# Optimization experiments

Measured on AMD Instinct MI355X. Metric: run time of the kernel, lower is better.

## Reference

```python
import jax, jax.numpy as jnp
import numpy as np
from jax import lax

GROUPS = 4
NEG_INF = -1000000000.0


def setup_inputs() -> dict:
    key = jax.random.key(0)
    k1, k2, k3 = jax.random.split(key, 3)
    B, C, L, K = 2, 16, 2048, 11
    scores = jax.random.normal(k1, (B, C, L, L), dtype=jnp.float32)
    weight = jax.random.normal(k2, (C, C // GROUPS, K, K), dtype=jnp.float32) * 0.05
    bias = jax.random.normal(k3, (C,), dtype=jnp.float32) * 0.05
    return {"scores": scores, "weight": weight, "bias": bias}


def reference(scores, weight, bias):
    B, C, L, _ = scores.shape
    K = weight.shape[-1]
    pad = K // 2
    # causal (lower-triangular) mask over the L x L score map
    mask = jnp.tril(jnp.ones((L, L), dtype=bool))[None, None]  # [1,1,L,L]
    neg_inf = jnp.asarray(NEG_INF, dtype=scores.dtype)
    s_inf = jnp.where(mask, scores, neg_inf)
    probs = jax.nn.softmax(s_inf, axis=-1)
    # grouped conv2d over the attention-probability maps, same padding
    out = lax.conv_general_dilated(
        probs, weight,
        window_strides=(1, 1),
        padding=[(pad, pad), (pad, pad)],
        dimension_numbers=("NCHW", "OIHW", "NCHW"),
        feature_group_count=GROUPS,
    )
    out = out + bias[None, :, None, None]
    # re-mask: zero out the upper triangle
    return jnp.where(mask, out, jnp.zeros((), dtype=out.dtype))
```

## Files before the change

kernel.cpp:

```cpp
#include <hip/hip_runtime.h>
#include <cmath>

#define L_DIM 2048
#define C_CH  16
#define B_SZ  2
#define N_G   4
#define C_PG  4
#define K_SZ  11

#define BX 64
#define BY 128
#define CHY 16
#define QROWS 31
#define QPITCH 84
#define QROWB (QPITCH*8)
#define NUNIT (QROWS*42)
#define NU 6
#define CXC 80
#define MP 52
#define CLWB (CXC*MP*2)

typedef _Float16 f16;
typedef __attribute__((ext_vector_type(2))) __fp16 fp16x2;
typedef __attribute__((ext_vector_type(8))) _Float16 f16x8;
typedef __attribute__((ext_vector_type(4))) float f32x4;
typedef unsigned long long u64;

struct alignas(8) H4 { f16 x, y, z, w; };
union H8U { H4 h[2]; uint4 u; };

__global__ void pack_w_k(const float* __restrict__ weight, u64* __restrict__ qprobs) {
  for (int e = threadIdx.x; e < 1536; e += 256) {
    const int l  = e & 63;
    const int r1 = e >> 6;
    const int t  = r1 % 3;
    const int r2 = r1 / 3;
    const int s  = r2 & 1;
    const int g  = r2 >> 1;
    const int m  = 16 * t + (l & 15);
    const int q  = l >> 4;
    const int kx = m >> 2, co = m & 3;
    f16 vals[8];
#pragma unroll
    for (int j = 0; j < 8; ++j) {
      const int ci = j & 3;
      const int ky = 8 * s + 2 * q + (j >> 2);
      float wv = 0.f;
      if (kx < K_SZ && ky < K_SZ)
        wv = weight[(((size_t)(g * 4 + co) * C_PG + ci) * K_SZ + ky) * K_SZ + kx];
      vals[j] = (f16)wv;
    }
    f16* dst = reinterpret_cast<f16*>(
        reinterpret_cast<char*>(qprobs) +
        ((size_t)(g * 2 + s) * L_DIM + 512) * 8 + (size_t)(t * 64 + l) * 16);
#pragma unroll
    for (int j = 0; j < 8; ++j) dst[j] = vals[j];
  }
}

__global__ __launch_bounds__(256) void softmax_q_k(
    const float* __restrict__ scores, u64* __restrict__ qprobs) {
  const int bid = blockIdx.x;
  const int zg  = bid & 7;
  const int y   = bid >> 3;
  const int b   = zg >> 2, g = zg & 3;
  const int tid = threadIdx.x;
  const int w    = tid >> 6;
  const int lane = tid & 63;

  __shared__ float mred[4][4];
  __shared__ float sred[4][4];

  const float* sbase = scores + ((size_t)(b * C_CH + g * 4) * L_DIM + y) * L_DIM;
  const size_t plane = (size_t)L_DIM * L_DIM;

  float v[4][8];
#pragma unroll
  for (int cc = 0; cc < 4; ++cc)
#pragma unroll
    for (int j = 0; j < 4; ++j) {
      const int x = 512 * w + 128 * j + 2 * lane;
      float2 f = make_float2(-INFINITY, -INFINITY);
      if (512 * w + 128 * j <= y) {
        f = *reinterpret_cast<const float2*>(sbase + cc * plane + x);
        if (x > y)     f.x = -INFINITY;
        if (x + 1 > y) f.y = -INFINITY;
      }
      v[cc][2 * j]     = f.x;
      v[cc][2 * j + 1] = f.y;
    }

  float ml[4];
#pragma unroll
  for (int cc = 0; cc < 4; ++cc) {
    float m = v[cc][0];
#pragma unroll
    for (int i = 1; i < 8; ++i) m = fmaxf(m, v[cc][i]);
#pragma unroll
    for (int off = 32; off >= 1; off >>= 1) m = fmaxf(m, __shfl_xor(m, off, 64));
    ml[cc] = m;
  }
  if (lane == 0) {
#pragma unroll
    for (int cc = 0; cc < 4; ++cc) mred[w][cc] = ml[cc];
  }
  __syncthreads();
  float mf[4];
#pragma unroll
  for (int cc = 0; cc < 4; ++cc)
    mf[cc] = fmaxf(fmaxf(mred[0][cc], mred[1][cc]),
                   fmaxf(mred[2][cc], mred[3][cc]));

  float sl[4];
#pragma unroll
  for (int cc = 0; cc < 4; ++cc) {
    float s = 0.f;
#pragma unroll
    for (int i = 0; i < 8; ++i) { v[cc][i] = __expf(v[cc][i] - mf[cc]); s += v[cc][i]; }
#pragma unroll
    for (int off = 32; off >= 1; off >>= 1) s += __shfl_xor(s, off, 64);
    sl[cc] = s;
  }
  if (lane == 0) {
#pragma unroll
    for (int cc = 0; cc < 4; ++cc) sred[w][cc] = sl[cc];
  }
  __syncthreads();
  float inv[4];
#pragma unroll
  for (int cc = 0; cc < 4; ++cc)
    inv[cc] = 1.0f / (sred[0][cc] + sred[1][cc] + sred[2][cc] + sred[3][cc]);

  u64* qrow = qprobs + ((size_t)zg * L_DIM + y) * L_DIM;
#pragma unroll
  for (int j = 0; j < 4; ++j) {
    const int xbase = 512 * w + 128 * j;
    if (xbase > y + 11) continue;
    const int x = xbase + 2 * lane;
    H8U o;
    o.h[0].x = (f16)(v[0][2*j]   * inv[0]);
    o.h[0].y = (f16)(v[1][2*j]   * inv[1]);
    o.h[0].z = (f16)(v[2][2*j]   * inv[2]);
    o.h[0].w = (f16)(v[3][2*j]   * inv[3]);
    o.h[1].x = (f16)(v[0][2*j+1] * inv[0]);
    o.h[1].y = (f16)(v[1][2*j+1] * inv[1]);
    o.h[1].z = (f16)(v[2][2*j+1] * inv[2]);
    o.h[1].w = (f16)(v[3][2*j+1] * inv[3]);
    *reinterpret_cast<uint4*>(qrow + x) = o.u;
  }
}

__global__ __launch_bounds__(256, 3) void conv_k(
    const u64* __restrict__ qprobs, const float* __restrict__ bias,
    float* __restrict__ out) {
  const int bid = blockIdx.x;
  const int zg  = bid & 7;
  const int lin = bid >> 3;
  const int xt  = lin & 31, yt = lin >> 5;
  const int x0 = xt * BX;
  const int Y0 = yt * BY;
  const int bb = zg >> 2, g = zg & 3;
  const int tid = threadIdx.x;
  const size_t plane = (size_t)L_DIM * L_DIM;

  float* outg = out + (size_t)(bb * C_CH + g * 4) * plane;

  if (x0 >= Y0 + BY) {
    const int co = (tid >> 4) & 3;
    const int xq = tid & 15;
    const float4 z4 = make_float4(0.f, 0.f, 0.f, 0.f);
    for (int r = (tid >> 6); r < BY; r += 4) {
      float* op = outg + (size_t)co * plane + (size_t)(Y0 + r) * L_DIM + x0 + 4 * xq;
      *reinterpret_cast<float4*>(op) = z4;
    }
    return;
  }

  __shared__ u64 Qs[QROWS * QPITCH];
  __shared__ f16 CLs[4 * CXC * MP];

  const int lane = tid & 63;
  const int w    = tid >> 6;
  const int q    = lane >> 4;
  const int c    = lane & 15;

  f16x8 A00, A01, A10, A11, A20, A21;
  {
    const char* qp0 = reinterpret_cast<const char*>(qprobs);
    const char* at0 = qp0 + ((size_t)(g * 2 + 0) * L_DIM + 512) * 8;
    const char* at1 = qp0 + ((size_t)(g * 2 + 1) * L_DIM + 512) * 8;
    A00 = *reinterpret_cast<const f16x8*>(at0 + (0 * 64 + lane) * 16);
    A10 = *reinterpret_cast<const f16x8*>(at0 + (1 * 64 + lane) * 16);
    A20 = *reinterpret_cast<const f16x8*>(at0 + (2 * 64 + lane) * 16);
    A01 = *reinterpret_cast<const f16x8*>(at1 + (0 * 64 + lane) * 16);
    A11 = *reinterpret_cast<const f16x8*>(at1 + (1 * 64 + lane) * 16);
    A21 = *reinterpret_cast<const f16x8*>(at1 + (2 * 64 + lane) * 16);
  }

  const float bs0 = bias[g * 4 + 0], bs1 = bias[g * 4 + 1];
  const float bs2 = bias[g * 4 + 2], bs3 = bias[g * 4 + 3];

  const u64* qplane = qprobs + (size_t)zg * plane;
  const int qx0 = x0 - 8;

  char* const qbase = reinterpret_cast<char*>(Qs);
  char* const clw   = reinterpret_cast<char*>(CLs) + w * CLWB;
  const char* const qlane = qbase + q * 1344 + c * 8;
  char* const clwr  = clw + c * 104 + q * 8;
  const char* const cle = clw + (lane + 3) * 104;

  for (int cb = Y0; cb < Y0 + BY; cb += CHY) {
    if (x0 > cb + CHY - 1) {
      const int co = (tid >> 4) & 3;
      const int xq = tid & 15;
      const float4 z4 = make_float4(0.f, 0.f, 0.f, 0.f);
      for (int r = (tid >> 6); r < CHY; r += 4) {
        float* op = outg + (size_t)co * plane + (size_t)(cb + r) * L_DIM + x0 + 4 * xq;
        *reinterpret_cast<float4*>(op) = z4;
      }
      continue;
    }

    uint4 sv[NU];
#pragma unroll
    for (int k = 0; k < NU; ++k) {
      const int u   = tid + 256 * k;
      const int r   = u / 42;
      const int c16 = u - 42 * r;
      const int py  = cb - 5 + r;
      const int qc0 = qx0 + 2 * c16;
      sv[k] = make_uint4(0u, 0u, 0u, 0u);
      if (u < NUNIT && py >= 0 && py < L_DIM && qc0 >= 0 && qc0 <= L_DIM - 2)
        sv[k] = *reinterpret_cast<const uint4*>(qplane + (size_t)py * L_DIM + qc0);
    }
    __syncthreads();
#pragma unroll
    for (int k = 0; k < NU; ++k) {
      const int u   = tid + 256 * k;
      if (u < NUNIT) {
        const int r   = u / 42;
        const int c16 = u - 42 * r;
        *reinterpret_cast<uint4*>(qbase + r * QROWB + c16 * 16) = sv[k];
      }
    }
    __syncthreads();

    for (int i = 0; i < CHY / 4; ++i) {
      const int y = cb + w * (CHY / 4) + i;
      float* orow = outg + (size_t)y * L_DIM + x0 + lane;
      if (y < x0) {
        orow[0] = 0.f; orow[plane] = 0.f;
        orow[2 * plane] = 0.f; orow[3 * plane] = 0.f;
        continue;
      }
      const char* qy = qlane + (y - cb) * QROWB;

      u64 b00[5], b01[5], b10[5], b11[5];
#pragma unroll
      for (int xs = 0; xs < 5; ++xs) {
        b00[xs] = *reinterpret_cast<const u64*>(qy + xs * 128 + 0);
        b01[xs] = *reinterpret_cast<const u64*>(qy + xs * 128 + 672);
        b10[xs] = *reinterpret_cast<const u64*>(qy + xs * 128 + 5376);
        b11[xs] = *reinterpret_cast<const u64*>(qy + xs * 128 + 6048);
      }

#pragma unroll
      for (int xs = 0; xs < 5; ++xs) {
        union { u64 u[2]; f16x8 v; } B0, B1;
        B0.u[0] = b00[xs]; B0.u[1] = b01[xs];
        B1.u[0] = b10[xs]; B1.u[1] = b11[xs];
        f32x4 z = {0.f, 0.f, 0.f, 0.f};
        f32x4 c0 = __builtin_amdgcn_mfma_f32_16x16x32_f16(A00, B0.v, z, 0, 0, 0);
        c0 = __builtin_amdgcn_mfma_f32_16x16x32_f16(A01, B1.v, c0, 0, 0, 0);
        f32x4 c1 = __builtin_amdgcn_mfma_f32_16x16x32_f16(A10, B0.v, z, 0, 0, 0);
        c1 = __builtin_amdgcn_mfma_f32_16x16x32_f16(A11, B1.v, c1, 0, 0, 0);
        f32x4 c2 = __builtin_amdgcn_mfma_f32_16x16x32_f16(A20, B0.v, z, 0, 0, 0);
        c2 = __builtin_amdgcn_mfma_f32_16x16x32_f16(A21, B1.v, c2, 0, 0, 0);

        union { fp16x2 h[2]; u64 u; } pk;
        pk.h[0] = __builtin_amdgcn_cvt_pkrtz(c0[0], c0[1]);
        pk.h[1] = __builtin_amdgcn_cvt_pkrtz(c0[2], c0[3]);
        *reinterpret_cast<u64*>(clwr + xs * 1664 + 0) = pk.u;
        pk.h[0] = __builtin_amdgcn_cvt_pkrtz(c1[0], c1[1]);
        pk.h[1] = __builtin_amdgcn_cvt_pkrtz(c1[2], c1[3]);
        *reinterpret_cast<u64*>(clwr + xs * 1664 + 32) = pk.u;
        pk.h[0] = __builtin_amdgcn_cvt_pkrtz(c2[0], c2[1]);
        pk.h[1] = __builtin_amdgcn_cvt_pkrtz(c2[2], c2[3]);
        *reinterpret_cast<u64*>(clwr + xs * 1664 + 64) = pk.u;
      }

      float s0 = 0.f, s1 = 0.f, s2 = 0.f, s3 = 0.f;
#pragma unroll
      for (int kx = 0; kx < K_SZ; ++kx) {
        union { u64 u; f16 h[4]; } cv;
        cv.u = *reinterpret_cast<const u64*>(cle + kx * 112);
        s0 += (float)cv.h[0]; s1 += (float)cv.h[1];
        s2 += (float)cv.h[2]; s3 += (float)cv.h[3];
      }
      const bool act = (x0 + lane) <= y;
      orow[0]         = act ? s0 + bs0 : 0.f;
      orow[plane]     = act ? s1 + bs1 : 0.f;
      orow[2 * plane] = act ? s2 + bs2 : 0.f;
      orow[3 * plane] = act ? s3 + bs3 : 0.f;
    }
  }
}

extern "C" void kernel_launch(void* const* d_in, const int* in_sizes, int n_in,
                              void* d_out, int out_size, void* d_ws, size_t ws_size,
                              hipStream_t stream) {
  const float* scores = (const float*)d_in[0];
  const float* weight = (const float*)d_in[1];
  const float* bias   = (const float*)d_in[2];
  float* outp = (float*)d_out;
  u64* qprobs = (u64*)d_ws;

  pack_w_k<<<1, 256, 0, stream>>>(weight, qprobs);

  softmax_q_k<<<B_SZ * N_G * L_DIM, 256, 0, stream>>>(scores, qprobs);

  conv_k<<<(L_DIM / BX) * (L_DIM / BY) * B_SZ * N_G, 256, 0, stream>>>(
      qprobs, bias, outp);
}
```

Measured before the change: 396.6 us.

## Store conv partials diagonally in LDS and reduce with vector loads in fp16

Changes the LDS layout of the per-wave MFMA partial results so each output column's 11 kx contributions sit contiguously along a skewed (diagonal) row. The epilogue can then gather them with a few wide 16-byte loads instead of 11 strided 8-byte loads, and sums them with packed fp16 adds. It also skips the redundant third-tile store for one lane quadrant and raises wave priority around the MFMA block. The trade-off is that accumulation in fp16 rather than fp32 loses precision.

```diff
diff --git a/kernel.cpp b/kernel.cpp
--- a/kernel.cpp
+++ b/kernel.cpp
@@ -16,9 +16,8 @@
 #define QROWB (QPITCH*8)
 #define NUNIT (QROWS*42)
 #define NU 6
-#define CXC 80
-#define MP 52
-#define CLWB (CXC*MP*2)
+#define DROWS 91
+#define DROWB 88
 
 typedef _Float16 f16;
 typedef __attribute__((ext_vector_type(2))) __fp16 fp16x2;
@@ -28,6 +27,9 @@
 
 struct alignas(8) H4 { f16 x, y, z, w; };
 union H8U { H4 h[2]; uint4 u; };
+union U32H2 { unsigned u; fp16x2 h; };
+
+__device__ __forceinline__ fp16x2 h2u(unsigned x) { U32H2 t; t.u = x; return t.h; }
 
 __global__ void pack_w_k(const float* __restrict__ weight, u64* __restrict__ qprobs) {
   for (int e = threadIdx.x; e < 1536; e += 256) {
@@ -177,7 +179,7 @@
   }
 
   __shared__ u64 Qs[QROWS * QPITCH];
-  __shared__ f16 CLs[4 * CXC * MP];
+  __shared__ u64 CLd[4 * DROWS * (DROWB/8)];
 
   const int lane = tid & 63;
   const int w    = tid >> 6;
@@ -204,10 +206,10 @@
   const int qx0 = x0 - 8;
 
   char* const qbase = reinterpret_cast<char*>(Qs);
-  char* const clw   = reinterpret_cast<char*>(CLs) + w * CLWB;
+  char* const clw   = reinterpret_cast<char*>(CLd) + w * (DROWS * DROWB);
   const char* const qlane = qbase + q * 1344 + c * 8;
-  char* const clwr  = clw + c * 104 + q * 8;
-  const char* const cle = clw + (lane + 3) * 104;
+  char* const cw = clw + (c - q + 11) * DROWB + q * 8;
+  const char* const ce = clw + (lane + 14) * DROWB;
 
   for (int cb = Y0; cb < Y0 + BY; cb += CHY) {
     if (x0 > cb + CHY - 1) {
@@ -236,7 +238,7 @@
     __syncthreads();
 #pragma unroll
     for (int k = 0; k < NU; ++k) {
-      const int u   = tid + 256 * k;
+      const int u = tid + 256 * k;
       if (u < NUNIT) {
         const int r   = u / 42;
         const int c16 = u - 42 * r;
@@ -264,6 +266,7 @@
         b11[xs] = *reinterpret_cast<const u64*>(qy + xs * 128 + 6048);
       }
 
+      __builtin_amdgcn_s_setprio(1);
 #pragma unroll
       for (int xs = 0; xs < 5; ++xs) {
         union { u64 u[2]; f16x8 v; } B0, B1;
@@ -280,28 +283,38 @@
         union { fp16x2 h[2]; u64 u; } pk;
         pk.h[0] = __builtin_amdgcn_cvt_pkrtz(c0[0], c0[1]);
         pk.h[1] = __builtin_amdgcn_cvt_pkrtz(c0[2], c0[3]);
-        *reinterpret_cast<u64*>(clwr + xs * 1664 + 0) = pk.u;
+        *reinterpret_cast<u64*>(cw + xs * 1408 + 0)   = pk.u;
         pk.h[0] = __builtin_amdgcn_cvt_pkrtz(c1[0], c1[1]);
         pk.h[1] = __builtin_amdgcn_cvt_pkrtz(c1[2], c1[3]);
-        *reinterpret_cast<u64*>(clwr + xs * 1664 + 32) = pk.u;
-        pk.h[0] = __builtin_amdgcn_cvt_pkrtz(c2[0], c2[1]);
-        pk.h[1] = __builtin_amdgcn_cvt_pkrtz(c2[2], c2[3]);
-        *reinterpret_cast<u64*>(clwr + xs * 1664 + 64) = pk.u;
-      }
-
-      float s0 = 0.f, s1 = 0.f, s2 = 0.f, s3 = 0.f;
-#pragma unroll
-      for (int kx = 0; kx < K_SZ; ++kx) {
-        union { u64 u; f16 h[4]; } cv;
-        cv.u = *reinterpret_cast<const u64*>(cle + kx * 112);
-        s0 += (float)cv.h[0]; s1 += (float)cv.h[1];
-        s2 += (float)cv.h[2]; s3 += (float)cv.h[3];
-      }
+        *reinterpret_cast<u64*>(cw + xs * 1408 - 320) = pk.u;
+        if (q != 3) {
+          pk.h[0] = __builtin_amdgcn_cvt_pkrtz(c2[0], c2[1]);
+          pk.h[1] = __builtin_amdgcn_cvt_pkrtz(c2[2], c2[3]);
+          *reinterpret_cast<u64*>(cw + xs * 1408 - 640) = pk.u;
+        }
+      }
+      __builtin_amdgcn_s_setprio(0);
+
+      const uint4 r0 = *reinterpret_cast<const uint4*>(ce + 0);
+      const uint4 r1 = *reinterpret_cast<const uint4*>(ce + 16);
+      const uint4 r2 = *reinterpret_cast<const uint4*>(ce + 32);
+      const uint4 r3 = *reinterpret_cast<const uint4*>(ce + 48);
+      const uint4 r4 = *reinterpret_cast<const uint4*>(ce + 64);
+      const uint2 r5 = *reinterpret_cast<const uint2*>(ce + 80);
+      fp16x2 e01 = (h2u(r0.x) + h2u(r0.z)) + (h2u(r1.x) + h2u(r1.z));
+      fp16x2 f01 = (h2u(r2.x) + h2u(r2.z)) + (h2u(r3.x) + h2u(r3.z));
+      fp16x2 g01 = (h2u(r4.x) + h2u(r4.z)) + h2u(r5.x);
+      e01 = (e01 + f01) + g01;
+      fp16x2 e23 = (h2u(r0.y) + h2u(r0.w)) + (h2u(r1.y) + h2u(r1.w));
+      fp16x2 f23 = (h2u(r2.y) + h2u(r2.w)) + (h2u(r3.y) + h2u(r3.w));
+      fp16x2 g23 = (h2u(r4.y) + h2u(r4.w)) + h2u(r5.y);
+      e23 = (e23 + f23) + g23;
+
       const bool act = (x0 + lane) <= y;
-      orow[0]         = act ? s0 + bs0 : 0.f;
-      orow[plane]     = act ? s1 + bs1 : 0.f;
-      orow[2 * plane] = act ? s2 + bs2 : 0.f;
-      orow[3 * plane] = act ? s3 + bs3 : 0.f;
+      orow[0]         = act ? (float)e01[0] + bs0 : 0.f;
+      orow[plane]     = act ? (float)e01[1] + bs1 : 0.f;
+      orow[2 * plane] = act ? (float)e23[0] + bs2 : 0.f;
+      orow[3 * plane] = act ? (float)e23[1] + bs3 : 0.f;
     }
   }
 }
```

Result: slower. 454.0 us (+14.5%).

## Load conv B operands directly from global memory, dropping LDS staging and barriers

Applied to the files above, without the earlier changes.

The conv kernel no longer stages a 31-row halo tile of packed probabilities into shared memory with two block barriers per 16-row chunk. Each wave now owns 32 consecutive output rows and loads its MFMA B operands straight from global memory, with a bounds-checked fallback for edge tiles. Launch bounds move from 3 to 4 blocks per CU now that LDS use is smaller. The trade is about 2.5x redundant global/L2 traffic from overlapping halo rows across row iterations, and uncoalesced 8-byte loads in place of 16-byte cooperative loads.

```diff
diff --git a/kernel.cpp b/kernel.cpp
--- a/kernel.cpp
+++ b/kernel.cpp
@@ -10,12 +10,6 @@
 
 #define BX 64
 #define BY 128
-#define CHY 16
-#define QROWS 31
-#define QPITCH 84
-#define QROWB (QPITCH*8)
-#define NUNIT (QROWS*42)
-#define NU 6
 #define CXC 80
 #define MP 52
 #define CLWB (CXC*MP*2)
@@ -150,7 +144,14 @@
   }
 }
 
-__global__ __launch_bounds__(256, 3) void conv_k(
+__device__ __forceinline__ u64 ldq(const u64* __restrict__ qplane, int row, int col) {
+  u64 v = 0;
+  if (((unsigned)row < (unsigned)L_DIM) && ((unsigned)col < (unsigned)L_DIM))
+    v = qplane[((size_t)row << 11) + col];
+  return v;
+}
+
+__global__ __launch_bounds__(256, 4) void conv_k(
     const u64* __restrict__ qprobs, const float* __restrict__ bias,
     float* __restrict__ out) {
   const int bid = blockIdx.x;
@@ -176,7 +177,6 @@
     return;
   }
 
-  __shared__ u64 Qs[QROWS * QPITCH];
   __shared__ f16 CLs[4 * CXC * MP];
 
   const int lane = tid & 63;
@@ -203,106 +203,81 @@
   const u64* qplane = qprobs + (size_t)zg * plane;
   const int qx0 = x0 - 8;
 
-  char* const qbase = reinterpret_cast<char*>(Qs);
-  char* const clw   = reinterpret_cast<char*>(CLs) + w * CLWB;
-  const char* const qlane = qbase + q * 1344 + c * 8;
-  char* const clwr  = clw + c * 104 + q * 8;
+  char* const clw  = reinterpret_cast<char*>(CLs) + w * CLWB;
+  char* const clwr = clw + c * 104 + q * 8;
   const char* const cle = clw + (lane + 3) * 104;
 
-  for (int cb = Y0; cb < Y0 + BY; cb += CHY) {
-    if (x0 > cb + CHY - 1) {
-      const int co = (tid >> 4) & 3;
-      const int xq = tid & 15;
-      const float4 z4 = make_float4(0.f, 0.f, 0.f, 0.f);
-      for (int r = (tid >> 6); r < CHY; r += 4) {
-        float* op = outg + (size_t)co * plane + (size_t)(cb + r) * L_DIM + x0 + 4 * xq;
-        *reinterpret_cast<float4*>(op) = z4;
+  const bool fastB = (x0 >= 8) && (x0 + 72 <= L_DIM);
+
+  for (int i = 0; i < 32; ++i) {
+    const int y = Y0 + 32 * w + i;
+    float* orow = outg + (size_t)y * L_DIM + x0 + lane;
+    if (y < x0) {
+      orow[0] = 0.f; orow[plane] = 0.f;
+      orow[2 * plane] = 0.f; orow[3 * plane] = 0.f;
+      continue;
+    }
+
+    u64 b00[5], b01[5], b10[5], b11[5];
+    const int py0 = y - 5 + 2 * q;
+    if (fastB && y <= L_DIM - 11) {
+      const u64* p0 = qplane + ((size_t)py0 << 11) + (qx0 + c);
+#pragma unroll
+      for (int xs = 0; xs < 5; ++xs) {
+        b00[xs] = p0[16 * xs];
+        b01[xs] = p0[16 * xs + 2048];
+        b10[xs] = p0[16 * xs + 16384];
+        b11[xs] = p0[16 * xs + 18432];
       }
-      continue;
-    }
-
-    uint4 sv[NU];
-#pragma unroll
-    for (int k = 0; k < NU; ++k) {
-      const int u   = tid + 256 * k;
-      const int r   = u / 42;
-      const int c16 = u - 42 * r;
-      const int py  = cb - 5 + r;
-      const int qc0 = qx0 + 2 * c16;
-      sv[k] = make_uint4(0u, 0u, 0u, 0u);
-      if (u < NUNIT && py >= 0 && py < L_DIM && qc0 >= 0 && qc0 <= L_DIM - 2)
-        sv[k] = *reinterpret_cast<const uint4*>(qplane + (size_t)py * L_DIM + qc0);
-    }
-    __syncthreads();
-#pragma unroll
-    for (int k = 0; k < NU; ++k) {
-      const int u   = tid + 256 * k;
-      if (u < NUNIT) {
-        const int r   = u / 42;
-        const int c16 = u - 42 * r;
-        *reinterpret_cast<uint4*>(qbase + r * QROWB + c16 * 16) = sv[k];
+    } else {
+#pragma unroll
+      for (int xs = 0; xs < 5; ++xs) {
+        const int col = qx0 + 16 * xs + c;
+        b00[xs] = ldq(qplane, py0,     col);
+        b01[xs] = ldq(qplane, py0 + 1, col);
+        b10[xs] = ldq(qplane, py0 + 8, col);
+        b11[xs] = ldq(qplane, py0 + 9, col);
       }
     }
-    __syncthreads();
-
-    for (int i = 0; i < CHY / 4; ++i) {
-      const int y = cb + w * (CHY / 4) + i;
-      float* orow = outg + (size_t)y * L_DIM + x0 + lane;
-      if (y < x0) {
-        orow[0] = 0.f; orow[plane] = 0.f;
-        orow[2 * plane] = 0.f; orow[3 * plane] = 0.f;
-        continue;
-      }
-      const char* qy = qlane + (y - cb) * QROWB;
-
-      u64 b00[5], b01[5], b10[5], b11[5];
-#pragma unroll
-      for (int xs = 0; xs < 5; ++xs) {
-        b00[xs] = *reinterpret_cast<const u64*>(qy + xs * 128 + 0);
-        b01[xs] = *reinterpret_cast<const u64*>(qy + xs * 128 + 672);
-        b10[xs] = *reinterpret_cast<const u64*>(qy + xs * 128 + 5376);
-        b11[xs] = *reinterpret_cast<const u64*>(qy + xs * 128 + 6048);
-      }
-
-#pragma unroll
-      for (int xs = 0; xs < 5; ++xs) {
-        union { u64 u[2]; f16x8 v; } B0, B1;
-        B0.u[0] = b00[xs]; B0.u[1] = b01[xs];
-        B1.u[0] = b10[xs]; B1.u[1] = b11[xs];
-        f32x4 z = {0.f, 0.f, 0.f, 0.f};
-        f32x4 c0 = __builtin_amdgcn_mfma_f32_16x16x32_f16(A00, B0.v, z, 0, 0, 0);
-        c0 = __builtin_amdgcn_mfma_f32_16x16x32_f16(A01, B1.v, c0, 0, 0, 0);
-        f32x4 c1 = __builtin_amdgcn_mfma_f32_16x16x32_f16(A10, B0.v, z, 0, 0, 0);
-        c1 = __builtin_amdgcn_mfma_f32_16x16x32_f16(A11, B1.v, c1, 0, 0, 0);
-        f32x4 c2 = __builtin_amdgcn_mfma_f32_16x16x32_f16(A20, B0.v, z, 0, 0, 0);
-        c2 = __builtin_amdgcn_mfma_f32_16x16x32_f16(A21, B1.v, c2, 0, 0, 0);
-
-        union { fp16x2 h[2]; u64 u; } pk;
-        pk.h[0] = __builtin_amdgcn_cvt_pkrtz(c0[0], c0[1]);
-        pk.h[1] = __builtin_amdgcn_cvt_pkrtz(c0[2], c0[3]);
-        *reinterpret_cast<u64*>(clwr + xs * 1664 + 0) = pk.u;
-        pk.h[0] = __builtin_amdgcn_cvt_pkrtz(c1[0], c1[1]);
-        pk.h[1] = __builtin_amdgcn_cvt_pkrtz(c1[2], c1[3]);
-        *reinterpret_cast<u64*>(clwr + xs * 1664 + 32) = pk.u;
-        pk.h[0] = __builtin_amdgcn_cvt_pkrtz(c2[0], c2[1]);
-        pk.h[1] = __builtin_amdgcn_cvt_pkrtz(c2[2], c2[3]);
-        *reinterpret_cast<u64*>(clwr + xs * 1664 + 64) = pk.u;
-      }
-
-      float s0 = 0.f, s1 = 0.f, s2 = 0.f, s3 = 0.f;
-#pragma unroll
-      for (int kx = 0; kx < K_SZ; ++kx) {
-        union { u64 u; f16 h[4]; } cv;
-        cv.u = *reinterpret_cast<const u64*>(cle + kx * 112);
-        s0 += (float)cv.h[0]; s1 += (float)cv.h[1];
-        s2 += (float)cv.h[2]; s3 += (float)cv.h[3];
-      }
-      const bool act = (x0 + lane) <= y;
-      orow[0]         = act ? s0 + bs0 : 0.f;
-      orow[plane]     = act ? s1 + bs1 : 0.f;
-      orow[2 * plane] = act ? s2 + bs2 : 0.f;
-      orow[3 * plane] = act ? s3 + bs3 : 0.f;
-    }
+
+#pragma unroll
+    for (int xs = 0; xs < 5; ++xs) {
+      union { u64 u[2]; f16x8 v; } B0, B1;
+      B0.u[0] = b00[xs]; B0.u[1] = b01[xs];
+      B1.u[0] = b10[xs]; B1.u[1] = b11[xs];
+      f32x4 z = {0.f, 0.f, 0.f, 0.f};
+      f32x4 c0 = __builtin_amdgcn_mfma_f32_16x16x32_f16(A00, B0.v, z, 0, 0, 0);
+      c0 = __builtin_amdgcn_mfma_f32_16x16x32_f16(A01, B1.v, c0, 0, 0, 0);
+      f32x4 c1 = __builtin_amdgcn_mfma_f32_16x16x32_f16(A10, B0.v, z, 0, 0, 0);
+      c1 = __builtin_amdgcn_mfma_f32_16x16x32_f16(A11, B1.v, c1, 0, 0, 0);
+      f32x4 c2 = __builtin_amdgcn_mfma_f32_16x16x32_f16(A20, B0.v, z, 0, 0, 0);
+      c2 = __builtin_amdgcn_mfma_f32_16x16x32_f16(A21, B1.v, c2, 0, 0, 0);
+
+      union { fp16x2 h[2]; u64 u; } pk;
+      pk.h[0] = __builtin_amdgcn_cvt_pkrtz(c0[0], c0[1]);
+      pk.h[1] = __builtin_amdgcn_cvt_pkrtz(c0[2], c0[3]);
+      *reinterpret_cast<u64*>(clwr + xs * 1664 + 0)  = pk.u;
+      pk.h[0] = __builtin_amdgcn_cvt_pkrtz(c1[0], c1[1]);
+      pk.h[1] = __builtin_amdgcn_cvt_pkrtz(c1[2], c1[3]);
+      *reinterpret_cast<u64*>(clwr + xs * 1664 + 32) = pk.u;
+      pk.h[0] = __builtin_amdgcn_cvt_pkrtz(c2[0], c2[1]);
+      pk.h[1] = __builtin_amdgcn_cvt_pkrtz(c2[2], c2[3]);
+      *reinterpret_cast<u64*>(clwr + xs * 1664 + 64) = pk.u;
+    }
+
+    float s0 = 0.f, s1 = 0.f, s2 = 0.f, s3 = 0.f;
+#pragma unroll
+    for (int kx = 0; kx < K_SZ; ++kx) {
+      union { u64 u; f16 h[4]; } cv;
+      cv.u = *reinterpret_cast<const u64*>(cle + kx * 112);
+      s0 += (float)cv.h[0]; s1 += (float)cv.h[1];
+      s2 += (float)cv.h[2]; s3 += (float)cv.h[3];
+    }
+    const bool act = (x0 + lane) <= y;
+    orow[0]         = act ? s0 + bs0 : 0.f;
+    orow[plane]     = act ? s1 + bs1 : 0.f;
+    orow[2 * plane] = act ? s2 + bs2 : 0.f;
+    orow[3 * plane] = act ? s3 + bs3 : 0.f;
   }
 }
 
```

Measured after the change: 508.8 us. 28.3% more time.
